# Kernel optimization log

Measured on AMD Instinct MI355X. Metric: run time of the kernel, lower is better.

The kernel has to match this reference:

```python
import jax, jax.numpy as jnp
import numpy as np

LAMBDA_TEMP = 20.0
GAMMA = 20.0
MARGIN = 0.05
EPS = 1e-8

B, K, M, D = 128, 256, 8, 128


def _unit(x, axis=-1):
    return x / jnp.linalg.norm(x, axis=axis, keepdims=True)


def setup_inputs() -> dict:
    key = jax.random.key(0)
    k1, k2, k3 = jax.random.split(key, 3)
    v_proj = _unit(jax.random.normal(k1, (B, K, D), dtype=jnp.float32))
    prototypes = _unit(jax.random.normal(k2, (K, M, D), dtype=jnp.float32))
    concept_labels = jax.random.randint(k3, (B, K), 0, 2, dtype=jnp.int64)
    return {"v_proj": v_proj, "concept_labels": concept_labels, "prototypes": prototypes}


def reference(v_proj, concept_labels, prototypes):
    # all-pairs prototype similarities: query vector (b,k) vs prototypes of concept c
    # sims: (B, K, C, M)
    sims = jnp.einsum('bkd,cmd->bkcm', v_proj, prototypes)
    # Eq.6: soft assignment over the M prototypes of each concept
    q = jax.nn.softmax(GAMMA * sims, axis=-1)
    # Eq.7-8: weighted similarity sim_c(v)  -> (B, K, C)
    sim = jnp.sum(q * sims, axis=-1)
    # positive similarity: concept k queried against its own prototypes, plus margin
    sim_pos = jnp.einsum('bkk->bk', sim) + MARGIN  # (B, K)
    # Eq.9: -log( exp(lam*sim_pos) / (sum_c exp(lam*sim_c) + eps) )
    denom = jnp.sum(jnp.exp(LAMBDA_TEMP * sim), axis=-1) + EPS  # (B, K)
    loss_bk = jnp.log(denom) - LAMBDA_TEMP * sim_pos  # (B, K)
    mask = (concept_labels == 1).astype(loss_bk.dtype)
    num_pos = jnp.sum(mask)
    total = jnp.sum(loss_bk * mask)
    return jnp.where(num_pos > 0, total / num_pos, total)
```

## Files before the change

kernel.cpp:

```cpp
#include <hip/hip_runtime.h>

#define LT      20.0f
#define LN2     0.69314718055994531f
#define C2EXP   28.853900817779268f
#define CHUNKS  16
#define NBLK    1024

typedef _Float16 half8  __attribute__((ext_vector_type(8)));
typedef float    f32x16 __attribute__((ext_vector_type(16)));

#if __has_builtin(__builtin_amdgcn_exp2f)
#define EXP2F(x) __builtin_amdgcn_exp2f(x)
#else
#define EXP2F(x) __expf(0.69314718055994531f * (x))
#endif

#define GLD16(gp, lp) __builtin_amdgcn_global_load_lds( \
    (const __attribute__((address_space(1))) void*)(gp), \
    (__attribute__((address_space(3))) void*)(lp), 16, 0, 0)


__global__ __launch_bounds__(1024)
void mpcl_prep_compact(const float* __restrict__ P,
                       const int*   __restrict__ labels,
                       _Float16* __restrict__ Pw,
                       int* __restrict__ ridx, int* __restrict__ npos)
{
    __shared__ int wcnt[512];
    __shared__ int wsum[8];
    __shared__ int sbase[512];
    __shared__ int tot;

    if (blockIdx.x < 32) {
        int t    = blockIdx.x * 1024 + threadIdx.x;
        int gcol = t >> 4;
        int dblk = t & 15;
        const float* src = P + ((size_t)gcol << 7) + dblk * 8;
        float4 x0 = *(const float4*)src;
        float4 x1 = *(const float4*)(src + 4);

        int ch = gcol >> 7, col = gcol & 127;
        int g  = col >> 5,  col5 = col & 31;
        int cl = col5 >> 3, p = col5 & 7;
        int a  = (p & 3) | ((cl & 1) << 2) | ((cl >> 1) << 3) | ((p >> 2) << 4);
        int hi = dblk & 1, s = dblk >> 1;
        int l  = (hi << 5) | a;
        int slot = ch * 2048 + (g * 8 + s) * 64 + l;

        half8 hv;
        hv[0] = (_Float16)(C2EXP * x0.x); hv[1] = (_Float16)(C2EXP * x0.y);
        hv[2] = (_Float16)(C2EXP * x0.z); hv[3] = (_Float16)(C2EXP * x0.w);
        hv[4] = (_Float16)(C2EXP * x1.x); hv[5] = (_Float16)(C2EXP * x1.y);
        hv[6] = (_Float16)(C2EXP * x1.z); hv[7] = (_Float16)(C2EXP * x1.w);
        *(half8*)(Pw + (size_t)slot * 8) = hv;
    } else {
        const int tid = threadIdx.x, lane = tid & 63, w = tid >> 6;
        int lab[32];
#pragma unroll
        for (int i = 0; i < 32; ++i) lab[i] = labels[i * 1024 + tid];
#pragma unroll
        for (int i = 0; i < 32; ++i) {
            unsigned long long m = __ballot(lab[i] == 1);
            if (lane == 0) wcnt[i * 16 + w] = __popcll(m);
        }
        __syncthreads();

        int v = 0, orig = 0;
        if (tid < 512) { v = wcnt[tid]; orig = v; }
#pragma unroll
        for (int off = 1; off < 64; off <<= 1) {
            int t2 = __shfl_up(v, off);
            if (lane >= off) v += t2;
        }
        if (lane == 63 && w < 8) wsum[w] = v;
        __syncthreads();
        if (tid == 0) {
            int acc = 0;
#pragma unroll
            for (int i = 0; i < 8; ++i) { int t2 = wsum[i]; wsum[i] = acc; acc += t2; }
            tot = acc; npos[0] = acc;
        }
        __syncthreads();
        if (tid < 512) sbase[tid] = v - orig + wsum[w];
        __syncthreads();

#pragma unroll
        for (int i = 0; i < 32; ++i) {
            unsigned long long m = __ballot(lab[i] == 1);
            int pos = sbase[i * 16 + w] + __popcll(m & ((1ull << lane) - 1));
            if (lab[i] == 1) ridx[pos] = i * 1024 + tid;
        }
        for (int j = tot + tid; j < 32768; j += 1024) ridx[j] = 0;
    }
}

__global__ __attribute__((amdgpu_flat_work_group_size(512, 512),
                          amdgpu_waves_per_eu(4, 4)))
void mpcl_main(const float* __restrict__ V,
               const _Float16* __restrict__ Pw,
               const int* __restrict__ ridx,
               const int* __restrict__ npos,
               float* __restrict__ part)
{
    __shared__ __align__(16) _Float16 Pst[8 * 4096];
    __shared__ float sh_denom[32];
    __shared__ float sh_simpos[32];

    const int np = *npos;
    const int rowbase = blockIdx.x * 32;
    if (rowbase >= np) return;

    const int tid = threadIdx.x;
    const int l   = tid & 63;
    const int w   = tid >> 6;
    const int g   = w & 3;
    const int kh  = w >> 2;
    const int a   = l & 31;
    const int hi  = l >> 5;

    if (tid < 32) sh_denom[tid] = 0.0f;

    const int pos   = rowbase + a;
    const int myrow = ridx[pos < np ? pos : np - 1];
    const int rowk  = myrow & 255;

    half8 vh[8];
    {
        const float* vr = V + ((size_t)myrow << 7) + hi * 8;
#pragma unroll
        for (int s = 0; s < 8; ++s) {
            float4 x0 = *(const float4*)(vr + s * 16);
            float4 x1 = *(const float4*)(vr + s * 16 + 4);
            vh[s][0] = (_Float16)x0.x; vh[s][1] = (_Float16)x0.y;
            vh[s][2] = (_Float16)x0.z; vh[s][3] = (_Float16)x0.w;
            vh[s][4] = (_Float16)x1.x; vh[s][5] = (_Float16)x1.y;
            vh[s][6] = (_Float16)x1.z; vh[s][7] = (_Float16)x1.w;
        }
    }
    __syncthreads();

    const _Float16* gbase = Pw + (size_t)g * 4096 + (size_t)l * 8;
    _Float16* lbase = &Pst[w * 4096];

#define STAGEH(CH, HF, B) do {                                        \
    const _Float16* g_ = gbase + (size_t)(CH) * 16384 + (HF) * 2048;  \
    _Float16* l_ = lbase + (B) * 2048;                                \
    GLD16(g_,        l_);        GLD16(g_ +  512, l_ +  512);         \
    GLD16(g_ + 1024, l_ + 1024); GLD16(g_ + 1536, l_ + 1536);         \
} while (0)

    const int ch0 = kh * 8;
    STAGEH(ch0, 0, 0);
    STAGEH(ch0, 1, 1);

    float dn = 0.f;

#define SOFT8(y0,y1,y2,y3,y4,y5,y6,y7, CONCEPT) do {                        \
    float e0=EXP2F(y0), e1=EXP2F(y1), e2=EXP2F(y2), e3=EXP2F(y3);           \
    float e4=EXP2F(y4), e5=EXP2F(y5), e6=EXP2F(y6), e7=EXP2F(y7);           \
    float es = ((e0+e1)+(e2+e3)) + ((e4+e5)+(e6+e7));                       \
    float ss = fmaf(e0,y0, fmaf(e1,y1, fmaf(e2,y2, e3*y3)))                 \
             + fmaf(e4,y4, fmaf(e5,y5, fmaf(e6,y6, e7*y7)));                \
    float simY = __fdividef(ss, es);                   \
    dn += EXP2F(simY);                                                      \
    if ((CONCEPT) == rowk) sh_simpos[a] = simY;      \
} while (0)

#pragma unroll 1
    for (int i = 0; i < 8; ++i) {
        const int ch = ch0 + i;

        f32x16 acA = {0.f,0.f,0.f,0.f,0.f,0.f,0.f,0.f,0.f,0.f,0.f,0.f,0.f,0.f,0.f,0.f};
        f32x16 acB = {0.f,0.f,0.f,0.f,0.f,0.f,0.f,0.f,0.f,0.f,0.f,0.f,0.f,0.f,0.f,0.f};

        asm volatile("s_waitcnt vmcnt(4)" ::: "memory");
        {
            const _Float16* bs = lbase;
            half8 p0 = *(const half8*)&bs[l * 8];
            half8 p1 = *(const half8*)&bs[l * 8 + 512];
            acA = __builtin_amdgcn_mfma_f32_32x32x16_f16(p0, vh[0], acA, 0, 0, 0);
            half8 p2 = *(const half8*)&bs[l * 8 + 1024];
            acA = __builtin_amdgcn_mfma_f32_32x32x16_f16(p1, vh[1], acA, 0, 0, 0);
            half8 p3 = *(const half8*)&bs[l * 8 + 1536];
            acA = __builtin_amdgcn_mfma_f32_32x32x16_f16(p2, vh[2], acA, 0, 0, 0);
            acA = __builtin_amdgcn_mfma_f32_32x32x16_f16(p3, vh[3], acA, 0, 0, 0);
        }
        asm volatile("s_waitcnt lgkmcnt(0)" ::: "memory");
        if (i + 1 < 8) STAGEH(ch + 1, 0, 0);

        if (i < 7) asm volatile("s_waitcnt vmcnt(4)" ::: "memory");
        else       asm volatile("s_waitcnt vmcnt(0)" ::: "memory");
        {
            const _Float16* bs = lbase + 2048;
            half8 p4 = *(const half8*)&bs[l * 8];
            half8 p5 = *(const half8*)&bs[l * 8 + 512];
            acB = __builtin_amdgcn_mfma_f32_32x32x16_f16(p4, vh[4], acB, 0, 0, 0);
            half8 p6 = *(const half8*)&bs[l * 8 + 1024];
            acB = __builtin_amdgcn_mfma_f32_32x32x16_f16(p5, vh[5], acB, 0, 0, 0);
            half8 p7 = *(const half8*)&bs[l * 8 + 1536];
            acB = __builtin_amdgcn_mfma_f32_32x32x16_f16(p6, vh[6], acB, 0, 0, 0);
            acB = __builtin_amdgcn_mfma_f32_32x32x16_f16(p7, vh[7], acB, 0, 0, 0);
        }
        asm volatile("s_waitcnt lgkmcnt(0)" ::: "memory");
        if (i + 1 < 8) STAGEH(ch + 1, 1, 1);

        f32x16 acc = acA + acB;
        const int cb = (ch << 4) + (g << 2) + hi;
        SOFT8(acc[0], acc[1], acc[2],  acc[3],  acc[8],  acc[9],  acc[10], acc[11], cb);
        SOFT8(acc[4], acc[5], acc[6],  acc[7],  acc[12], acc[13], acc[14], acc[15], cb + 2);
    }

    {
        float t = dn;
        t += __shfl_xor(t, 32);
        if (hi == 0)
            atomicAdd(&sh_denom[a], t);
    }
    __syncthreads();

    if (w == 0) {
        float s = 0.f, cc = 0.f;
        if (l < 32 && rowbase + l < np) {
            s  = logf(sh_denom[l] + 1e-8f) - LN2 * sh_simpos[l] - 1.0f;
            cc = 1.0f;
        }
#pragma unroll
        for (int off = 32; off >= 1; off >>= 1) {
            s  += __shfl_down(s, off);
            cc += __shfl_down(cc, off);
        }
        if (l == 0) {
            part[2 * blockIdx.x]     = s;
            part[2 * blockIdx.x + 1] = cc;
        }
    }
}

__global__ __launch_bounds__(512)
void mpcl_finish(const float* __restrict__ part, const int* __restrict__ npos,
                 float* __restrict__ out)
{
    __shared__ float sh[16];
    const int tid  = threadIdx.x;
    const int lane = tid & 63;
    const int w    = tid >> 6;
    const int nact = (*npos + 31) >> 5;

    float s = 0.f, cc = 0.f;
    for (int i = tid; i < nact; i += 512) {
        s  += part[2 * i];
        cc += part[2 * i + 1];
    }
#pragma unroll
    for (int off = 32; off >= 1; off >>= 1) {
        s  += __shfl_down(s, off);
        cc += __shfl_down(cc, off);
    }
    if (lane == 0) { sh[w] = s; sh[8 + w] = cc; }
    __syncthreads();
    if (tid == 0) {
        float ts = 0.f, tc = 0.f;
#pragma unroll
        for (int i = 0; i < 8; ++i) { ts += sh[i]; tc += sh[8 + i]; }
        out[0] = (tc > 0.0f) ? (ts / tc) : ts;
    }
}

extern "C" void kernel_launch(void* const* d_in, const int* in_sizes, int n_in,
                              void* d_out, int out_size, void* d_ws, size_t ws_size,
                              hipStream_t stream)
{
    const float* V      = (const float*)d_in[0];
    const int*   labels = (const int*)d_in[1];
    const float* P      = (const float*)d_in[2];
    float* out = (float*)d_out;

    int*      npos = (int*)d_ws;
    float*    part = (float*)((char*)d_ws + 256);
    int*      ridx = (int*)((char*)d_ws + 16384);
    _Float16* Pw   = (_Float16*)((char*)d_ws + 147456);

    mpcl_prep_compact<<<33, 1024, 0, stream>>>(P, labels, Pw, ridx, npos);
    mpcl_main<<<NBLK, 512, 0, stream>>>(V, Pw, ridx, npos, part);
    mpcl_finish<<<1, 512, 0, stream>>>(part, npos, out);
}
```

Measured before the change: 94.50 us.

## Process two 32-row query tiles per block to reuse staged prototype loads

Each block now handles 64 compacted positive rows instead of 32, holding two sets of query fragments in registers and issuing two MFMA chains per prototype fragment read from LDS. This halves the number of blocks and the total prototype staging traffic per row, and interleaves independent accumulators to hide MFMA latency. Register pressure doubles for the V fragments and accumulators, so occupancy is lowered to 2 waves per EU, which may reduce latency hiding and cut parallelism to fewer blocks.

```diff
diff --git a/kernel.cpp b/kernel.cpp
--- a/kernel.cpp
+++ b/kernel.cpp
@@ -4,7 +4,7 @@
 #define LN2     0.69314718055994531f
 #define C2EXP   28.853900817779268f
 #define CHUNKS  16
-#define NBLK    1024
+#define NBLK    512
 
 typedef _Float16 half8  __attribute__((ext_vector_type(8)));
 typedef float    f32x16 __attribute__((ext_vector_type(16)));
@@ -95,7 +95,7 @@
 }
 
 __global__ __attribute__((amdgpu_flat_work_group_size(512, 512),
-                          amdgpu_waves_per_eu(4, 4)))
+                          amdgpu_waves_per_eu(2, 2)))
 void mpcl_main(const float* __restrict__ V,
                const _Float16* __restrict__ Pw,
                const int* __restrict__ ridx,
@@ -103,11 +103,11 @@
                float* __restrict__ part)
 {
     __shared__ __align__(16) _Float16 Pst[8 * 4096];
-    __shared__ float sh_denom[32];
-    __shared__ float sh_simpos[32];
+    __shared__ float sh_denom[64];
+    __shared__ float sh_simpos[64];
 
     const int np = *npos;
-    const int rowbase = blockIdx.x * 32;
+    const int rowbase = blockIdx.x * 64;
     if (rowbase >= np) return;
 
     const int tid = threadIdx.x;
@@ -118,23 +118,24 @@
     const int a   = l & 31;
     const int hi  = l >> 5;
 
-    if (tid < 32) sh_denom[tid] = 0.0f;
-
-    const int pos   = rowbase + a;
-    const int myrow = ridx[pos < np ? pos : np - 1];
-    const int rowk  = myrow & 255;
-
-    half8 vh[8];
-    {
-        const float* vr = V + ((size_t)myrow << 7) + hi * 8;
+    if (tid < 64) { sh_denom[tid] = 0.0f; sh_simpos[tid] = 0.0f; }
+
+    int myrow[2], rowk[2];
+    half8 vh[2][8];
+#pragma unroll
+    for (int rf = 0; rf < 2; ++rf) {
+        int pos = rowbase + rf * 32 + a;
+        myrow[rf] = ridx[pos < np ? pos : np - 1];
+        rowk[rf]  = myrow[rf] & 255;
+        const float* vr = V + ((size_t)myrow[rf] << 7) + hi * 8;
 #pragma unroll
         for (int s = 0; s < 8; ++s) {
             float4 x0 = *(const float4*)(vr + s * 16);
             float4 x1 = *(const float4*)(vr + s * 16 + 4);
-            vh[s][0] = (_Float16)x0.x; vh[s][1] = (_Float16)x0.y;
-            vh[s][2] = (_Float16)x0.z; vh[s][3] = (_Float16)x0.w;
-            vh[s][4] = (_Float16)x1.x; vh[s][5] = (_Float16)x1.y;
-            vh[s][6] = (_Float16)x1.z; vh[s][7] = (_Float16)x1.w;
+            vh[rf][s][0] = (_Float16)x0.x; vh[rf][s][1] = (_Float16)x0.y;
+            vh[rf][s][2] = (_Float16)x0.z; vh[rf][s][3] = (_Float16)x0.w;
+            vh[rf][s][4] = (_Float16)x1.x; vh[rf][s][5] = (_Float16)x1.y;
+            vh[rf][s][6] = (_Float16)x1.z; vh[rf][s][7] = (_Float16)x1.w;
         }
     }
     __syncthreads();
@@ -153,37 +154,41 @@
     STAGEH(ch0, 0, 0);
     STAGEH(ch0, 1, 1);
 
-    float dn = 0.f;
-
-#define SOFT8(y0,y1,y2,y3,y4,y5,y6,y7, CONCEPT) do {                        \
+    float dn0 = 0.f, dn1 = 0.f;
+
+#define SOFT8(y0,y1,y2,y3,y4,y5,y6,y7, CONCEPT, DN, SLOT) do {              \
     float e0=EXP2F(y0), e1=EXP2F(y1), e2=EXP2F(y2), e3=EXP2F(y3);           \
     float e4=EXP2F(y4), e5=EXP2F(y5), e6=EXP2F(y6), e7=EXP2F(y7);           \
     float es = ((e0+e1)+(e2+e3)) + ((e4+e5)+(e6+e7));                       \
     float ss = fmaf(e0,y0, fmaf(e1,y1, fmaf(e2,y2, e3*y3)))                 \
              + fmaf(e4,y4, fmaf(e5,y5, fmaf(e6,y6, e7*y7)));                \
     float simY = __fdividef(ss, es);                   \
-    dn += EXP2F(simY);                                                      \
-    if ((CONCEPT) == rowk) sh_simpos[a] = simY;      \
+    DN += EXP2F(simY);                                                      \
+    if ((CONCEPT) == rowk[(SLOT) >> 5]) sh_simpos[SLOT] = simY;             \
 } while (0)
 
 #pragma unroll 1
     for (int i = 0; i < 8; ++i) {
         const int ch = ch0 + i;
 
-        f32x16 acA = {0.f,0.f,0.f,0.f,0.f,0.f,0.f,0.f,0.f,0.f,0.f,0.f,0.f,0.f,0.f,0.f};
-        f32x16 acB = {0.f,0.f,0.f,0.f,0.f,0.f,0.f,0.f,0.f,0.f,0.f,0.f,0.f,0.f,0.f,0.f};
+        f32x16 ac0 = {0.f,0.f,0.f,0.f,0.f,0.f,0.f,0.f,0.f,0.f,0.f,0.f,0.f,0.f,0.f,0.f};
+        f32x16 ac1 = {0.f,0.f,0.f,0.f,0.f,0.f,0.f,0.f,0.f,0.f,0.f,0.f,0.f,0.f,0.f,0.f};
 
         asm volatile("s_waitcnt vmcnt(4)" ::: "memory");
         {
             const _Float16* bs = lbase;
             half8 p0 = *(const half8*)&bs[l * 8];
             half8 p1 = *(const half8*)&bs[l * 8 + 512];
-            acA = __builtin_amdgcn_mfma_f32_32x32x16_f16(p0, vh[0], acA, 0, 0, 0);
             half8 p2 = *(const half8*)&bs[l * 8 + 1024];
-            acA = __builtin_amdgcn_mfma_f32_32x32x16_f16(p1, vh[1], acA, 0, 0, 0);
             half8 p3 = *(const half8*)&bs[l * 8 + 1536];
-            acA = __builtin_amdgcn_mfma_f32_32x32x16_f16(p2, vh[2], acA, 0, 0, 0);
-            acA = __builtin_amdgcn_mfma_f32_32x32x16_f16(p3, vh[3], acA, 0, 0, 0);
+            ac0 = __builtin_amdgcn_mfma_f32_32x32x16_f16(p0, vh[0][0], ac0, 0, 0, 0);
+            ac1 = __builtin_amdgcn_mfma_f32_32x32x16_f16(p0, vh[1][0], ac1, 0, 0, 0);
+            ac0 = __builtin_amdgcn_mfma_f32_32x32x16_f16(p1, vh[0][1], ac0, 0, 0, 0);
+            ac1 = __builtin_amdgcn_mfma_f32_32x32x16_f16(p1, vh[1][1], ac1, 0, 0, 0);
+            ac0 = __builtin_amdgcn_mfma_f32_32x32x16_f16(p2, vh[0][2], ac0, 0, 0, 0);
+            ac1 = __builtin_amdgcn_mfma_f32_32x32x16_f16(p2, vh[1][2], ac1, 0, 0, 0);
+            ac0 = __builtin_amdgcn_mfma_f32_32x32x16_f16(p3, vh[0][3], ac0, 0, 0, 0);
+            ac1 = __builtin_amdgcn_mfma_f32_32x32x16_f16(p3, vh[1][3], ac1, 0, 0, 0);
         }
         asm volatile("s_waitcnt lgkmcnt(0)" ::: "memory");
         if (i + 1 < 8) STAGEH(ch + 1, 0, 0);
@@ -194,33 +199,40 @@
             const _Float16* bs = lbase + 2048;
             half8 p4 = *(const half8*)&bs[l * 8];
             half8 p5 = *(const half8*)&bs[l * 8 + 512];
-            acB = __builtin_amdgcn_mfma_f32_32x32x16_f16(p4, vh[4], acB, 0, 0, 0);
             half8 p6 = *(const half8*)&bs[l * 8 + 1024];
-            acB = __builtin_amdgcn_mfma_f32_32x32x16_f16(p5, vh[5], acB, 0, 0, 0);
             half8 p7 = *(const half8*)&bs[l * 8 + 1536];
-            acB = __builtin_amdgcn_mfma_f32_32x32x16_f16(p6, vh[6], acB, 0, 0, 0);
-            acB = __builtin_amdgcn_mfma_f32_32x32x16_f16(p7, vh[7], acB, 0, 0, 0);
+            ac0 = __builtin_amdgcn_mfma_f32_32x32x16_f16(p4, vh[0][4], ac0, 0, 0, 0);
+            ac1 = __builtin_amdgcn_mfma_f32_32x32x16_f16(p4, vh[1][4], ac1, 0, 0, 0);
+            ac0 = __builtin_amdgcn_mfma_f32_32x32x16_f16(p5, vh[0][5], ac0, 0, 0, 0);
+            ac1 = __builtin_amdgcn_mfma_f32_32x32x16_f16(p5, vh[1][5], ac1, 0, 0, 0);
+            ac0 = __builtin_amdgcn_mfma_f32_32x32x16_f16(p6, vh[0][6], ac0, 0, 0, 0);
+            ac1 = __builtin_amdgcn_mfma_f32_32x32x16_f16(p6, vh[1][6], ac1, 0, 0, 0);
+            ac0 = __builtin_amdgcn_mfma_f32_32x32x16_f16(p7, vh[0][7], ac0, 0, 0, 0);
+            ac1 = __builtin_amdgcn_mfma_f32_32x32x16_f16(p7, vh[1][7], ac1, 0, 0, 0);
         }
         asm volatile("s_waitcnt lgkmcnt(0)" ::: "memory");
         if (i + 1 < 8) STAGEH(ch + 1, 1, 1);
 
-        f32x16 acc = acA + acB;
         const int cb = (ch << 4) + (g << 2) + hi;
-        SOFT8(acc[0], acc[1], acc[2],  acc[3],  acc[8],  acc[9],  acc[10], acc[11], cb);
-        SOFT8(acc[4], acc[5], acc[6],  acc[7],  acc[12], acc[13], acc[14], acc[15], cb + 2);
+        SOFT8(ac0[0], ac0[1], ac0[2],  ac0[3],  ac0[8],  ac0[9],  ac0[10], ac0[11], cb,     dn0, a);
+        SOFT8(ac0[4], ac0[5], ac0[6],  ac0[7],  ac0[12], ac0[13], ac0[14], ac0[15], cb + 2, dn0, a);
+        SOFT8(ac1[0], ac1[1], ac1[2],  ac1[3],  ac1[8],  ac1[9],  ac1[10], ac1[11], cb,     dn1, 32 + a);
+        SOFT8(ac1[4], ac1[5], ac1[6],  ac1[7],  ac1[12], ac1[13], ac1[14], ac1[15], cb + 2, dn1, 32 + a);
     }
 
     {
-        float t = dn;
-        t += __shfl_xor(t, 32);
-        if (hi == 0)
-            atomicAdd(&sh_denom[a], t);
+        float t0 = dn0 + __shfl_xor(dn0, 32);
+        float t1 = dn1 + __shfl_xor(dn1, 32);
+        if (hi == 0) {
+            atomicAdd(&sh_denom[a],      t0);
+            atomicAdd(&sh_denom[32 + a], t1);
+        }
     }
     __syncthreads();
 
     if (w == 0) {
         float s = 0.f, cc = 0.f;
-        if (l < 32 && rowbase + l < np) {
+        if (rowbase + l < np) {
             s  = logf(sh_denom[l] + 1e-8f) - LN2 * sh_simpos[l] - 1.0f;
             cc = 1.0f;
         }
@@ -244,7 +256,7 @@
     const int tid  = threadIdx.x;
     const int lane = tid & 63;
     const int w    = tid >> 6;
-    const int nact = (*npos + 31) >> 5;
+    const int nact = (*npos + 63) >> 6;
 
     float s = 0.f, cc = 0.f;
     for (int i = tid; i < nact; i += 512) {
```

Result: no change. 93.56 us (-1.0%).
